# Performance work log

Measured on AMD Instinct MI355X. Metric: run time of the kernel, lower is better.

## Reference

```python
import jax, jax.numpy as jnp
import numpy as np

EMPHASIS_FACTOR = 1.5

def setup_inputs() -> dict:
    key = jax.random.key(0)
    k1, k2 = jax.random.split(key)
    B, T, F = 32, 4096, 256
    x = jax.random.normal(k1, (B, T, F), dtype=jnp.float32)
    W = jax.random.normal(k2, (F, 1), dtype=jnp.float32) * (1.0 / np.sqrt(F))
    b = jnp.zeros((1,), dtype=jnp.float32)
    return {"x": x, "W": W, "b": b}

def reference(x, W, b):
    # x: [B, T, F], W: [F, 1], b: [1]
    B, T, F = x.shape
    e = jnp.tanh(x @ W + b)                 # [B, T, 1]
    a = jax.nn.softmax(e, axis=1)           # softmax over time
    a_flat = a[..., 0]                      # [B, T]
    k = max(1, int(T * 0.1))
    _, top_idx = jax.lax.top_k(a_flat, k)   # [B, k]
    # scatter True at top-k positions (instead of O(T*k) broadcast compare)
    mask = jnp.zeros((B, T), dtype=bool).at[jnp.arange(B)[:, None], top_idx].set(True)
    a_emph = jnp.where(mask[..., None], a * EMPHASIS_FACTOR, a)  # [B, T, 1]
    return jnp.sum(x * a_emph, axis=1, keepdims=True)            # [B, 1, F]
```

## Files before the change

### kernel.cpp

```cpp
#include <hip/hip_runtime.h>
#include <math.h>

#define BB 32
#define TT 4096
#define FF 256
#define K_TOP 409
#define EMPH 1.5f

__global__ void zero_kernel(float* __restrict__ p, int n) {
    int i = blockIdx.x * 256 + threadIdx.x;
    if (i < n) p[i] = 0.f;
}

__global__ __launch_bounds__(256) void dot_tanh_kernel(const float* __restrict__ x,
                                                       const float* __restrict__ W,
                                                       const float* __restrict__ bias,
                                                       float* __restrict__ e) {
    const int wave = threadIdx.x >> 6;
    const int lane = threadIdx.x & 63;
    const size_t bt = (size_t)blockIdx.x * 4 + wave;

    const float4* xv = (const float4*)(x + bt * FF);
    const float4* wv = (const float4*)W;
    const float4 xe = xv[lane];
    const float4 we = wv[lane];
    float d = xe.x * we.x + xe.y * we.y + xe.z * we.z + xe.w * we.w;

    #pragma unroll
    for (int off = 32; off; off >>= 1) d += __shfl_down(d, off);

    if (lane == 0) e[bt] = tanhf(d + bias[0]);
}

__global__ __launch_bounds__(256) void softmax_select_kernel(const float* __restrict__ e,
                                                             float* __restrict__ w) {
    const int b = blockIdx.x;
    const int tid = threadIdx.x;
    const int wave = tid >> 6, lane = tid & 63;
    const float* eb = e + (size_t)b * TT;

    float ev[16];
    unsigned key[16];
    float lmax = -1e30f;
    #pragma unroll
    for (int j = 0; j < 16; j++) {
        float v = eb[tid + 256 * j];
        ev[j] = v;
        unsigned u = __float_as_uint(v);
        key[j] = (u & 0x80000000u) ? ~u : (u | 0x80000000u);
        lmax = fmaxf(lmax, v);
    }

    __shared__ float sf[4];
    __shared__ int   sc[4];

    #pragma unroll
    for (int off = 32; off; off >>= 1) lmax = fmaxf(lmax, __shfl_down(lmax, off));
    if (lane == 0) sf[wave] = lmax;
    __syncthreads();
    const float emax = fmaxf(fmaxf(sf[0], sf[1]), fmaxf(sf[2], sf[3]));
    __syncthreads();

    float pe[16];
    float lsum = 0.f;
    #pragma unroll
    for (int j = 0; j < 16; j++) { pe[j] = expf(ev[j] - emax); lsum += pe[j]; }
    #pragma unroll
    for (int off = 32; off; off >>= 1) lsum += __shfl_down(lsum, off);
    if (lane == 0) sf[wave] = lsum;
    __syncthreads();
    const float sumexp = sf[0] + sf[1] + sf[2] + sf[3];

    unsigned prefix = 0u, mask = 0u;
    int kk = K_TOP;
    for (int bit = 31; bit >= 0; bit--) {
        const unsigned bm = 1u << bit;
        const unsigned m2 = mask | bm;
        const unsigned want = prefix | bm;
        int c = 0;
        #pragma unroll
        for (int j = 0; j < 16; j++) c += (int)((key[j] & m2) == want);
        #pragma unroll
        for (int off = 32; off; off >>= 1) c += __shfl_down(c, off);
        __syncthreads();
        if (lane == 0) sc[wave] = c;
        __syncthreads();
        const int tot = sc[0] + sc[1] + sc[2] + sc[3];
        if (tot >= kk) prefix = want; else kk -= tot;
        mask = m2;
    }
    const unsigned Kkey = prefix;

    const float inv = 1.f / sumexp;
    float* wb = w + (size_t)b * TT;
    #pragma unroll
    for (int j = 0; j < 16; j++) {
        float val = pe[j] * inv;
        if (key[j] >= Kkey) val *= EMPH;
        wb[tid + 256 * j] = val;
    }
}

#define CHUNK 128
__global__ __launch_bounds__(256) void wsum_kernel(const float* __restrict__ x,
                                                   const float* __restrict__ w,
                                                   float* __restrict__ out) {
    const int chunks = TT / CHUNK;
    const int b  = blockIdx.x / chunks;
    const int c0 = (blockIdx.x % chunks) * CHUNK;
    const int wave = threadIdx.x >> 6, lane = threadIdx.x & 63;

    const float4* xb = (const float4*)(x + ((size_t)b * TT + c0) * FF);
    const float*  wb = w + (size_t)b * TT + c0;

    float4 acc = make_float4(0.f, 0.f, 0.f, 0.f);
    for (int t = wave; t < CHUNK; t += 4) {
        const float  wt = wb[t];
        const float4 xe = xb[t * 64 + lane];
        acc.x += xe.x * wt; acc.y += xe.y * wt;
        acc.z += xe.z * wt; acc.w += xe.w * wt;
    }

    __shared__ float4 part4[4][64];
    part4[wave][lane] = acc;
    __syncthreads();

    const float* pf = (const float*)part4;
    const float s = pf[threadIdx.x] + pf[256 + threadIdx.x] +
                    pf[512 + threadIdx.x] + pf[768 + threadIdx.x];
    atomicAdd(&out[b * FF + threadIdx.x], s);
}

extern "C" void kernel_launch(void* const* d_in, const int* in_sizes, int n_in,
                              void* d_out, int out_size, void* d_ws, size_t ws_size,
                              hipStream_t stream) {
    const float* x    = (const float*)d_in[0];
    const float* W    = (const float*)d_in[1];
    const float* bias = (const float*)d_in[2];
    float* out = (float*)d_out;

    float* e = (float*)d_ws;
    float* w = e + (size_t)BB * TT;

    zero_kernel<<<(BB * FF + 255) / 256, 256, 0, stream>>>(out, BB * FF);
    dot_tanh_kernel<<<BB * TT / 4, 256, 0, stream>>>(x, W, bias, e);
    softmax_select_kernel<<<BB, 256, 0, stream>>>(e, w);
    wsum_kernel<<<BB * (TT / CHUNK), 256, 0, stream>>>(x, w, out);
}
```

Baseline: 222.0 us.

## Fuse score and online-softmax weighted sum into one pass over x

Computes tanh scores and an online-softmax weighted partial sum per 64-timestep chunk in a single read of x, storing per-chunk max, sum and partial vectors. A small select kernel finds the top-k threshold and the global normaliser, and a combine kernel rescales the chunk partials and adds the extra 0.5 weight only for the selected timesteps by re-reading just those rows of x. This removes the second full pass over the 128MB input, at the cost of extra partial buffers and a scattered gather of the top-k rows.

New measurement: 217.9 us. Within noise of the previous version (-1.9%).

```diff
diff --git a/kernel.cpp b/kernel.cpp
--- a/kernel.cpp
+++ b/kernel.cpp
@@ -4,72 +4,131 @@
 #define BB 32
 #define TT 4096
 #define FF 256
+#define CH 64
+#define NC (TT / CH)
+#define ST 16
 #define K_TOP 409
-#define EMPH 1.5f
+#define NSEG 16
+#define SEGT (TT / NSEG)
+#define CPS (NC / NSEG)
+
+__device__ __forceinline__ unsigned flip_key(float v) {
+    unsigned u = __float_as_uint(v);
+    return (u & 0x80000000u) ? ~u : (u | 0x80000000u);
+}
 
 __global__ void zero_kernel(float* __restrict__ p, int n) {
     int i = blockIdx.x * 256 + threadIdx.x;
     if (i < n) p[i] = 0.f;
 }
 
-__global__ __launch_bounds__(256) void dot_tanh_kernel(const float* __restrict__ x,
-                                                       const float* __restrict__ W,
-                                                       const float* __restrict__ bias,
-                                                       float* __restrict__ e) {
-    const int wave = threadIdx.x >> 6;
-    const int lane = threadIdx.x & 63;
-    const size_t bt = (size_t)blockIdx.x * 4 + wave;
-
-    const float4* xv = (const float4*)(x + bt * FF);
-    const float4* wv = (const float4*)W;
-    const float4 xe = xv[lane];
-    const float4 we = wv[lane];
-    float d = xe.x * we.x + xe.y * we.y + xe.z * we.z + xe.w * we.w;
-
-    #pragma unroll
-    for (int off = 32; off; off >>= 1) d += __shfl_down(d, off);
-
-    if (lane == 0) e[bt] = tanhf(d + bias[0]);
-}
-
-__global__ __launch_bounds__(256) void softmax_select_kernel(const float* __restrict__ e,
-                                                             float* __restrict__ w) {
+__global__ __launch_bounds__(256) void fused_pass1(const float* __restrict__ x,
+                                                   const float* __restrict__ W,
+                                                   const float* __restrict__ bias,
+                                                   float* __restrict__ e,
+                                                   float* __restrict__ P,
+                                                   float* __restrict__ cm,
+                                                   float* __restrict__ cs) {
+    const int b = blockIdx.x / NC;
+    const int c = blockIdx.x % NC;
+    const int tid = threadIdx.x;
+    const int wv = tid >> 6, ln = tid & 63;
+
+    const float* xc = x + ((size_t)b * TT + (size_t)c * CH) * FF;
+    const float4 wvec = ((const float4*)W)[ln];
+    const float  bb   = bias[0];
+
+    __shared__ float se[ST];
+    __shared__ float4 part4[4][64];
+    __shared__ float swsum[4];
+
+    float4 acc = make_float4(0.f, 0.f, 0.f, 0.f);
+    float  m = -1e30f, ssum = 0.f;
+
+    for (int s0 = 0; s0 < CH; s0 += ST) {
+        float4 xr[4];
+        #pragma unroll
+        for (int i = 0; i < 4; i++) {
+            const int tl = s0 + wv * 4 + i;
+            xr[i] = ((const float4*)(xc + (size_t)tl * FF))[ln];
+        }
+        float dv[4];
+        #pragma unroll
+        for (int i = 0; i < 4; i++)
+            dv[i] = xr[i].x * wvec.x + xr[i].y * wvec.y +
+                    xr[i].z * wvec.z + xr[i].w * wvec.w;
+        #pragma unroll
+        for (int i = 0; i < 4; i++) {
+            float d = dv[i];
+            #pragma unroll
+            for (int off = 32; off; off >>= 1) d += __shfl_xor(d, off);
+            dv[i] = tanhf(d + bb);
+        }
+        __syncthreads();
+        if (ln == 0) {
+            #pragma unroll
+            for (int i = 0; i < 4; i++) {
+                se[wv * 4 + i] = dv[i];
+                e[(size_t)b * TT + c * CH + s0 + wv * 4 + i] = dv[i];
+            }
+        }
+        __syncthreads();
+
+        float lm = m;
+        #pragma unroll
+        for (int i = 0; i < ST; i++) lm = fmaxf(lm, se[i]);
+        const float alpha = __expf(m - lm);
+        acc.x *= alpha; acc.y *= alpha; acc.z *= alpha; acc.w *= alpha;
+        ssum *= alpha;
+        #pragma unroll
+        for (int i = 0; i < 4; i++) {
+            const float wgt = __expf(dv[i] - lm);
+            ssum += wgt;
+            acc.x += wgt * xr[i].x; acc.y += wgt * xr[i].y;
+            acc.z += wgt * xr[i].z; acc.w += wgt * xr[i].w;
+        }
+        m = lm;
+    }
+
+    part4[wv][ln] = acc;
+    if (ln == 0) swsum[wv] = ssum;
+    __syncthreads();
+    const float* pf = (const float*)part4;
+    const float p = pf[tid] + pf[256 + tid] + pf[512 + tid] + pf[768 + tid];
+    P[((size_t)b * NC + c) * FF + tid] = p;
+    if (tid == 0) {
+        cm[b * NC + c] = m;
+        cs[b * NC + c] = swsum[0] + swsum[1] + swsum[2] + swsum[3];
+    }
+}
+
+__global__ __launch_bounds__(256) void select_kernel(const float* __restrict__ e,
+                                                     const float* __restrict__ cm,
+                                                     const float* __restrict__ cs,
+                                                     float* __restrict__ stats) {
     const int b = blockIdx.x;
     const int tid = threadIdx.x;
-    const int wave = tid >> 6, lane = tid & 63;
+    const int wv = tid >> 6, ln = tid & 63;
+
+    __shared__ float sgm, sZ;
+    __shared__ int sc[4];
+
+    if (tid < 64) {
+        const float mm = cm[b * NC + tid];
+        const float ss = cs[b * NC + tid];
+        float g = mm;
+        #pragma unroll
+        for (int off = 32; off; off >>= 1) g = fmaxf(g, __shfl_xor(g, off));
+        float zz = ss * __expf(mm - g);
+        #pragma unroll
+        for (int off = 32; off; off >>= 1) zz += __shfl_xor(zz, off);
+        if (tid == 0) { sgm = g; sZ = zz; }
+    }
+
     const float* eb = e + (size_t)b * TT;
-
-    float ev[16];
     unsigned key[16];
-    float lmax = -1e30f;
     #pragma unroll
-    for (int j = 0; j < 16; j++) {
-        float v = eb[tid + 256 * j];
-        ev[j] = v;
-        unsigned u = __float_as_uint(v);
-        key[j] = (u & 0x80000000u) ? ~u : (u | 0x80000000u);
-        lmax = fmaxf(lmax, v);
-    }
-
-    __shared__ float sf[4];
-    __shared__ int   sc[4];
-
-    #pragma unroll
-    for (int off = 32; off; off >>= 1) lmax = fmaxf(lmax, __shfl_down(lmax, off));
-    if (lane == 0) sf[wave] = lmax;
-    __syncthreads();
-    const float emax = fmaxf(fmaxf(sf[0], sf[1]), fmaxf(sf[2], sf[3]));
-    __syncthreads();
-
-    float pe[16];
-    float lsum = 0.f;
-    #pragma unroll
-    for (int j = 0; j < 16; j++) { pe[j] = expf(ev[j] - emax); lsum += pe[j]; }
-    #pragma unroll
-    for (int off = 32; off; off >>= 1) lsum += __shfl_down(lsum, off);
-    if (lane == 0) sf[wave] = lsum;
-    __syncthreads();
-    const float sumexp = sf[0] + sf[1] + sf[2] + sf[3];
+    for (int j = 0; j < 16; j++) key[j] = flip_key(eb[tid + 256 * j]);
 
     unsigned prefix = 0u, mask = 0u;
     int kk = K_TOP;
@@ -77,58 +136,70 @@
         const unsigned bm = 1u << bit;
         const unsigned m2 = mask | bm;
         const unsigned want = prefix | bm;
-        int c = 0;
-        #pragma unroll
-        for (int j = 0; j < 16; j++) c += (int)((key[j] & m2) == want);
-        #pragma unroll
-        for (int off = 32; off; off >>= 1) c += __shfl_down(c, off);
-        __syncthreads();
-        if (lane == 0) sc[wave] = c;
+        int cnt = 0;
+        #pragma unroll
+        for (int j = 0; j < 16; j++) cnt += (int)((key[j] & m2) == want);
+        #pragma unroll
+        for (int off = 32; off; off >>= 1) cnt += __shfl_down(cnt, off);
+        __syncthreads();
+        if (ln == 0) sc[wv] = cnt;
         __syncthreads();
         const int tot = sc[0] + sc[1] + sc[2] + sc[3];
         if (tot >= kk) prefix = want; else kk -= tot;
         mask = m2;
     }
-    const unsigned Kkey = prefix;
-
-    const float inv = 1.f / sumexp;
-    float* wb = w + (size_t)b * TT;
+
+    if (tid == 0) {
+        stats[3 * b + 0] = sgm;
+        stats[3 * b + 1] = sZ;
+        stats[3 * b + 2] = __uint_as_float(prefix);
+    }
+}
+
+__global__ __launch_bounds__(256) void combine_kernel(const float* __restrict__ x,
+                                                      const float* __restrict__ e,
+                                                      const float* __restrict__ P,
+                                                      const float* __restrict__ cm,
+                                                      const float* __restrict__ stats,
+                                                      float* __restrict__ out) {
+    const int b = blockIdx.x / NSEG;
+    const int s = blockIdx.x % NSEG;
+    const int tid = threadIdx.x;
+
+    const float gmax = stats[3 * b + 0];
+    const float Z    = stats[3 * b + 1];
+    const unsigned Kkey = __float_as_uint(stats[3 * b + 2]);
+
+    float acc = 0.f;
     #pragma unroll
-    for (int j = 0; j < 16; j++) {
-        float val = pe[j] * inv;
-        if (key[j] >= Kkey) val *= EMPH;
-        wb[tid + 256 * j] = val;
-    }
-}
-
-#define CHUNK 128
-__global__ __launch_bounds__(256) void wsum_kernel(const float* __restrict__ x,
-                                                   const float* __restrict__ w,
-                                                   float* __restrict__ out) {
-    const int chunks = TT / CHUNK;
-    const int b  = blockIdx.x / chunks;
-    const int c0 = (blockIdx.x % chunks) * CHUNK;
-    const int wave = threadIdx.x >> 6, lane = threadIdx.x & 63;
-
-    const float4* xb = (const float4*)(x + ((size_t)b * TT + c0) * FF);
-    const float*  wb = w + (size_t)b * TT + c0;
-
-    float4 acc = make_float4(0.f, 0.f, 0.f, 0.f);
-    for (int t = wave; t < CHUNK; t += 4) {
-        const float  wt = wb[t];
-        const float4 xe = xb[t * 64 + lane];
-        acc.x += xe.x * wt; acc.y += xe.y * wt;
-        acc.z += xe.z * wt; acc.w += xe.w * wt;
-    }
-
-    __shared__ float4 part4[4][64];
-    part4[wave][lane] = acc;
+    for (int c = 0; c < CPS; c++) {
+        const int cc = s * CPS + c;
+        const float sc2 = __expf(cm[b * NC + cc] - gmax);
+        acc += P[((size_t)b * NC + cc) * FF + tid] * sc2;
+    }
+
+    __shared__ int scount;
+    __shared__ int slist[SEGT];
+    __shared__ float sval[SEGT];
+    if (tid == 0) scount = 0;
     __syncthreads();
 
-    const float* pf = (const float*)part4;
-    const float s = pf[threadIdx.x] + pf[256 + threadIdx.x] +
-                    pf[512 + threadIdx.x] + pf[768 + threadIdx.x];
-    atomicAdd(&out[b * FF + threadIdx.x], s);
+    const int t = s * SEGT + tid;
+    const float ev = e[(size_t)b * TT + t];
+    if (flip_key(ev) >= Kkey) {
+        const int i = atomicAdd(&scount, 1);
+        slist[i] = t;
+        sval[i] = ev;
+    }
+    __syncthreads();
+
+    const int n = scount;
+    for (int i = 0; i < n; i++) {
+        const float coeff = 0.5f * __expf(sval[i] - gmax);
+        acc += coeff * x[((size_t)b * TT + slist[i]) * FF + tid];
+    }
+
+    atomicAdd(&out[b * FF + tid], acc / Z);
 }
 
 extern "C" void kernel_launch(void* const* d_in, const int* in_sizes, int n_in,
@@ -139,11 +210,14 @@
     const float* bias = (const float*)d_in[2];
     float* out = (float*)d_out;
 
-    float* e = (float*)d_ws;
-    float* w = e + (size_t)BB * TT;
+    float* e     = (float*)d_ws;
+    float* P     = e + (size_t)BB * TT;
+    float* cm    = P + (size_t)BB * NC * FF;
+    float* cs    = cm + BB * NC;
+    float* stats = cs + BB * NC;
 
     zero_kernel<<<(BB * FF + 255) / 256, 256, 0, stream>>>(out, BB * FF);
-    dot_tanh_kernel<<<BB * TT / 4, 256, 0, stream>>>(x, W, bias, e);
-    softmax_select_kernel<<<BB, 256, 0, stream>>>(e, w);
-    wsum_kernel<<<BB * (TT / CHUNK), 256, 0, stream>>>(x, w, out);
-}
+    fused_pass1<<<BB * NC, 256, 0, stream>>>(x, W, bias, e, P, cm, cs);
+    select_kernel<<<BB, 256, 0, stream>>>(e, cm, cs, stats);
+    combine_kernel<<<BB * NSEG, 256, 0, stream>>>(x, e, P, cm, stats, out);
+}
```
